# Kernel optimization log

Hardware: AMD Instinct MI355X
Metric: run time of the kernel (lower is better)

## Reference

```python
import jax, jax.numpy as jnp
import numpy as np

N = 100000
E = 3200000


def setup_inputs() -> dict:
    key = jax.random.key(0)
    ks = jax.random.split(key, 12)
    x = jax.random.normal(ks[0], (N, 124), dtype=jnp.float32)
    pos = jax.random.normal(ks[1], (N, 3), dtype=jnp.float32)
    z = jax.random.normal(ks[2], (N,), dtype=jnp.float32)
    edge_index = jax.random.randint(ks[3], (2, E), 0, N, dtype=jnp.int64)
    def lin(k, fin, fout):
        kw, kb = jax.random.split(k)
        s = 1.0 / np.sqrt(fin)
        W = jax.random.uniform(kw, (fin, fout), minval=-s, maxval=s, dtype=jnp.float32)
        b = jax.random.uniform(kb, (fout,), minval=-s, maxval=s, dtype=jnp.float32)
        return W, b
    W1, b1 = lin(ks[4], 128, 256)
    W2, b2 = lin(ks[5], 256, 256)
    W3, b3 = lin(ks[6], 256, 256)
    W4, b4 = lin(ks[7], 256, 1)
    return {"x": x, "pos": pos, "z": z, "edge_index": edge_index,
            "W1": W1, "b1": b1, "W2": W2, "b2": b2,
            "W3": W3, "b3": b3, "W4": W4, "b4": b4}


def reference(x, pos, z, edge_index, W1, b1, W2, b2, W3, b3, W4, b4):
    # features = hstack(x, pos, z[:, None])  -> [N, input_dim]
    feats = jnp.concatenate([x, pos, z[:, None]], axis=1)
    src, dst = edge_index[0], edge_index[1]
    # sum of neighbor (dst) features into each src node: O(E) segment-sum
    sums = jax.ops.segment_sum(feats[dst], src, num_segments=feats.shape[0])
    # per-node L2 normalize (matches torch.linalg.norm per row)
    h = sums / jnp.linalg.norm(sums, axis=1, keepdims=True)
    h = jax.nn.relu(h @ W1 + b1)
    h = jax.nn.relu(h @ W2 + b2)
    h = jax.nn.relu(h @ W3 + b3)
    h = h @ W4 + b4            # [N, 1]
    return jnp.mean(h, axis=0)  # [1]
```

## Files before the change

kernel.cpp:

```cpp
#include <hip/hip_runtime.h>
#include <math.h>

#define N_NODES 100000
#define N_EDGES 3200000
#define BSHIFT 6
#define NBUCK 1563
#define NBLK_E 256
#define EPB 12500
#define CAP 3072

typedef _Float16 half8 __attribute__((ext_vector_type(8)));
typedef float f32x4 __attribute__((ext_vector_type(4)));
typedef float f32x2 __attribute__((ext_vector_type(2)));

__device__ __forceinline__ void gload16(const void* gsrc, void* ldst) {
    __builtin_amdgcn_global_load_lds(
        (const __attribute__((address_space(1))) unsigned int*)gsrc,
        (__attribute__((address_space(3))) unsigned int*)ldst,
        16, 0, 0);
}

__global__ __launch_bounds__(256) void pack_kernel(
    const float* __restrict__ x, const float* __restrict__ pos,
    const float* __restrict__ z, unsigned int* __restrict__ feats8)
{
    int idx = blockIdx.x * blockDim.x + threadIdx.x;
    if (idx >= N_NODES * 32) return;
    int n = idx >> 5, j = idx & 31;
    float v[4];
    #pragma unroll
    for (int k = 0; k < 4; ++k) {
        int f = j * 4 + k;
        if (f < 124)      v[k] = x[n * 124 + f];
        else if (f < 127) v[k] = pos[n * 3 + (f - 124)];
        else              v[k] = z[n];
    }
    int u = 0;
    u = __builtin_amdgcn_cvt_pk_fp8_f32(v[0], v[1], u, false);
    u = __builtin_amdgcn_cvt_pk_fp8_f32(v[2], v[3], u, true);
    feats8[idx] = (unsigned int)u;
}

__global__ __launch_bounds__(256) void wprep_kernel(
    const float* __restrict__ W, int K, _Float16* __restrict__ WT)
{
    int idx = blockIdx.x * blockDim.x + threadIdx.x;
    if (idx >= K * 256) return;
    int k = idx >> 8, c = idx & 255;
    WT[c * K + k] = (_Float16)W[idx];
}

__global__ __launch_bounds__(1024) void coarse_hist_kernel(
    const int* __restrict__ ei, int* __restrict__ gcnt)
{
    __shared__ int bins[NBUCK];
    int t = threadIdx.x, blk = blockIdx.x;
    for (int b = t; b < NBUCK; b += 1024) bins[b] = 0;
    __syncthreads();
    int base = blk * EPB;
    for (int i = t; i < EPB; i += 1024) {
        int src = __builtin_nontemporal_load(&ei[base + i]);
        atomicAdd(&bins[src >> BSHIFT], 1);
    }
    __syncthreads();
    for (int b = t; b < NBUCK; b += 1024)
        gcnt[blk * NBUCK + b] = bins[b];
}

__global__ __launch_bounds__(256) void bucket_tot_kernel(
    const int* __restrict__ gcnt, int* __restrict__ btot)
{
    __shared__ int red[4];
    int b = blockIdx.x, t = threadIdx.x;
    int s = gcnt[t * NBUCK + b];
    #pragma unroll
    for (int off = 32; off > 0; off >>= 1) s += __shfl_xor(s, off, 64);
    if ((t & 63) == 0) red[t >> 6] = s;
    __syncthreads();
    if (t == 0) btot[b] = red[0] + red[1] + red[2] + red[3];
}

__global__ __launch_bounds__(1024) void scan_buckets_kernel(
    const int* __restrict__ btot, int* __restrict__ bbase)
{
    __shared__ int s[1024];
    int t = threadIdx.x;
    int i0 = 2 * t, i1 = 2 * t + 1;
    int v0 = (i0 < NBUCK) ? btot[i0] : 0;
    int v1 = (i1 < NBUCK) ? btot[i1] : 0;
    int sum = v0 + v1;
    s[t] = sum;
    __syncthreads();
    for (int off = 1; off < 1024; off <<= 1) {
        int o = (t >= off) ? s[t - off] : 0;
        __syncthreads();
        s[t] += o;
        __syncthreads();
    }
    int excl = s[t] - sum;
    if (i0 < NBUCK) bbase[i0] = excl;
    if (i1 < NBUCK) bbase[i1] = excl + v0;
    if (i0 == NBUCK - 1) bbase[NBUCK] = excl + v0;
    if (i1 == NBUCK - 1) bbase[NBUCK] = excl + v0 + v1;
}

__global__ __launch_bounds__(256) void colscan_kernel(
    const int* __restrict__ gcnt, const int* __restrict__ bbase,
    int* __restrict__ gbase)
{
    __shared__ int s[NBLK_E];
    int b = blockIdx.x, t = threadIdx.x;
    int v = gcnt[t * NBUCK + b];
    s[t] = v;
    __syncthreads();
    for (int off = 1; off < NBLK_E; off <<= 1) {
        int o = (t >= off) ? s[t - off] : 0;
        __syncthreads();
        s[t] += o;
        __syncthreads();
    }
    gbase[t * NBUCK + b] = bbase[b] + s[t] - v;
}

__global__ __launch_bounds__(1024) void bucket_scatter_kernel(
    const int* __restrict__ ei, const int* __restrict__ gcnt,
    const int* __restrict__ gbase, unsigned int* __restrict__ bucketed)
{
    __shared__ unsigned int val[EPB];
    __shared__ int gd[EPB];
    __shared__ int cur[NBUCK];
    __shared__ int gofs[NBUCK];
    __shared__ int ssum[1024];

    int t = threadIdx.x, blk = blockIdx.x;

    int i0 = 2 * t, i1 = 2 * t + 1;
    int c0 = (i0 < NBUCK) ? gcnt[blk * NBUCK + i0] : 0;
    int c1 = (i1 < NBUCK) ? gcnt[blk * NBUCK + i1] : 0;
    int sum = c0 + c1;
    ssum[t] = sum;
    __syncthreads();
    for (int off = 1; off < 1024; off <<= 1) {
        int o = (t >= off) ? ssum[t - off] : 0;
        __syncthreads();
        ssum[t] += o;
        __syncthreads();
    }
    int excl = ssum[t] - sum;
    if (i0 < NBUCK) { cur[i0] = excl;      gofs[i0] = gbase[blk * NBUCK + i0] - excl; }
    if (i1 < NBUCK) { cur[i1] = excl + c0; gofs[i1] = gbase[blk * NBUCK + i1] - (excl + c0); }
    __syncthreads();

    int base = blk * EPB;
    for (int i = t; i < EPB; i += 1024) {
        int e = base + i;
        int src = __builtin_nontemporal_load(&ei[e]);
        int dst = __builtin_nontemporal_load(&ei[N_EDGES + e]);
        int b = src >> BSHIFT;
        int r = atomicAdd(&cur[b], 1);
        val[r] = (unsigned int)dst | ((unsigned int)(src & 63) << 17);
        gd[r] = gofs[b] + r;
    }
    __syncthreads();

    for (int i = t; i < EPB; i += 1024)
        bucketed[gd[i]] = val[i];
}

__global__ __launch_bounds__(256) void sortagg_kernel(
    const int* __restrict__ bbase, const unsigned int* __restrict__ bucketed,
    const unsigned int* __restrict__ feats8, _Float16* __restrict__ h0)
{
    __shared__ unsigned int srt[CAP];
    __shared__ int excl[64], cur[64];

    int t = threadIdx.x, b = blockIdx.x;
    int segs = bbase[b], cnt = bbase[b + 1] - segs;
    if (cnt > CAP) cnt = CAP;

    if (t < 64) cur[t] = 0;
    __syncthreads();

    for (int i = t; i < cnt; i += 256)
        atomicAdd(&cur[(bucketed[segs + i] >> 17) & 63], 1);
    __syncthreads();

    int v = (t < 64) ? cur[t] : 0;
    if (t < 64) excl[t] = v;
    __syncthreads();
    for (int off = 1; off < 64; off <<= 1) {
        int o = (t >= off && t < 64) ? excl[t - off] : 0;
        __syncthreads();
        if (t < 64) excl[t] += o;
        __syncthreads();
    }
    if (t < 64) { excl[t] -= v; cur[t] = excl[t]; }
    __syncthreads();

    for (int i = t; i < cnt; i += 256) {
        unsigned int p = bucketed[segs + i];
        int r = atomicAdd(&cur[(p >> 17) & 63], 1);
        if (r < CAP) srt[r] = p & 0x1FFFFu;
    }
    __syncthreads();

    int w = t >> 6, lane = t & 63;
    int h = lane >> 5, s = lane & 31;
    const unsigned int* fb = feats8 + s;

#define ACC4(U)                                                     \
    a01 += __builtin_amdgcn_cvt_pk_f32_fp8((U), false);             \
    a23 += __builtin_amdgcn_cvt_pk_f32_fp8((U), true);

    for (int j = 0; j < 16; ++j) {
        int nl = w * 16 + j;
        int node = b * 64 + nl;
        if (node >= N_NODES) break;
        int start = excl[nl], end = cur[nl];
        f32x2 a01 = {0.f, 0.f}, a23 = {0.f, 0.f};
        int i = start;
        for (; i + 24 <= end; i += 24) {
            unsigned int uu[12];
            #pragma unroll
            for (int q = 0; q < 12; ++q)
                uu[q] = fb[(long long)srt[i + 2 * q + h] * 32];
            #pragma unroll
            for (int q = 0; q < 12; ++q) { ACC4(uu[q]); }
        }
        for (; i + 8 <= end; i += 8) {
            unsigned int uu[4];
            #pragma unroll
            for (int q = 0; q < 4; ++q)
                uu[q] = fb[(long long)srt[i + 2 * q + h] * 32];
            #pragma unroll
            for (int q = 0; q < 4; ++q) { ACC4(uu[q]); }
        }
        for (; i + 2 <= end; i += 2) {
            unsigned int u = fb[(long long)srt[i + h] * 32];
            ACC4(u);
        }
        if (i < end && h == 0) {
            unsigned int u = fb[(long long)srt[i] * 32];
            ACC4(u);
        }
        float a0 = a01[0], a1 = a01[1], a2 = a23[0], a3 = a23[1];
        a0 += __shfl_xor(a0, 32, 64);
        a1 += __shfl_xor(a1, 32, 64);
        a2 += __shfl_xor(a2, 32, 64);
        a3 += __shfl_xor(a3, 32, 64);
        float ss = a0 * a0 + a1 * a1 + a2 * a2 + a3 * a3;
        #pragma unroll
        for (int off = 16; off > 0; off >>= 1) ss += __shfl_xor(ss, off, 64);
        float inv = 1.0f / sqrtf(ss);
        if (h == 0) {
            union { uint2 u; _Float16 f[4]; } o;
            o.f[0] = (_Float16)(a0 * inv); o.f[1] = (_Float16)(a1 * inv);
            o.f[2] = (_Float16)(a2 * inv); o.f[3] = (_Float16)(a3 * inv);
            *reinterpret_cast<uint2*>(&h0[(long long)node * 128 + s * 4]) = o.u;
        }
    }
#undef ACC4
}

__global__ __launch_bounds__(256, 2) void fused_mlp_kernel(
    const _Float16* __restrict__ h0,
    const _Float16* __restrict__ WT1,
    const float* __restrict__ b1,
    const _Float16* __restrict__ WT2,
    const float* __restrict__ b2,
    const _Float16* __restrict__ WT3,
    const float* __restrict__ b3,
    const float* __restrict__ W4,
    float* __restrict__ partials, int M)
{
    __shared__ __align__(16) _Float16 sA[8 * 2048];
    __shared__ __align__(16) _Float16 sB[3][8192];

    const int t = threadIdx.x;
    const int row0 = blockIdx.x * 64;

    const int ar = t >> 2, ap = t & 3;
    const int ag = ap ^ ((ar >> 1) & 3);
    int arow = row0 + ar; if (arow > M - 1) arow = M - 1;
    const _Float16* aSrc = h0 + (long long)arow * 128 + ag * 8;

    const int bc0 = t >> 2;
    const int gb = ap ^ ((bc0 >> 1) & 3);

    const int w = t >> 6, lane = t & 63;
    const int wr = w >> 1, wc = w & 1;
    const int lrow = lane & 15, g = lane >> 4;

    unsigned int offA[2], offB[8];
    #pragma unroll
    for (int rt = 0; rt < 2; ++rt) {
        int r = wr * 32 + rt * 16 + lrow;
        offA[rt] = r * 64 + (g ^ ((r >> 1) & 3)) * 16;
    }
    #pragma unroll
    for (int ct = 0; ct < 8; ++ct) {
        int cidx = wc * 128 + ct * 16 + lrow;
        offB[ct] = cidx * 64 + (g ^ ((cidx >> 1) & 3)) * 16;
    }

    float bb1[8], bb2[8], bb3[8], w4v[8];
    #pragma unroll
    for (int ct = 0; ct < 8; ++ct) {
        int col = wc * 128 + ct * 16 + lrow;
        bb1[ct] = b1[col]; bb2[ct] = b2[col];
        bb3[ct] = b3[col]; w4v[ct] = W4[col];
    }

    f32x4 acc[2][8];
    #pragma unroll
    for (int i = 0; i < 2; ++i)
        #pragma unroll
        for (int j = 0; j < 8; ++j)
            acc[i][j] = (f32x4){0.f, 0.f, 0.f, 0.f};

#define STG(WT, Kv, KC, BUF)                                                 \
    {                                                                        \
        _Pragma("unroll")                                                    \
        for (int j = 0; j < 4; ++j)                                          \
            gload16((WT) + (long long)(bc0 + j * 64) * (Kv) + gb * 8 +       \
                        (KC) * 32,                                           \
                    (char*)sB[BUF] + j * 4096 + t * 16);                     \
    }

#define WB(N)                                                                \
    asm volatile("s_waitcnt vmcnt(" #N ")" ::: "memory");                    \
    __builtin_amdgcn_s_barrier();                                            \
    __builtin_amdgcn_sched_barrier(0);

#define EB() __builtin_amdgcn_s_barrier();

#define SEAM()                                                               \
    asm volatile("s_waitcnt lgkmcnt(0)" ::: "memory");                       \
    __builtin_amdgcn_s_barrier();                                            \
    __builtin_amdgcn_sched_barrier(0);

#define STORE_ACTS(BB)                                                       \
    {                                                                        \
        _Pragma("unroll")                                                    \
        for (int ct = 0; ct < 8; ++ct) {                                     \
            int col = wc * 128 + ct * 16 + lrow;                             \
            float bb = (BB)[ct];                                             \
            int chk = col >> 5, kk = col & 31;                               \
            int kg = kk >> 3, ke = kk & 7;                                   \
            _Pragma("unroll")                                                \
            for (int rt = 0; rt < 2; ++rt) {                                 \
                _Pragma("unroll")                                            \
                for (int jj = 0; jj < 4; ++jj) {                             \
                    int rowl = wr * 32 + rt * 16 + g * 4 + jj;               \
                    int slot = kg ^ ((rowl >> 1) & 3);                       \
                    sA[chk * 2048 + rowl * 32 + slot * 8 + ke] =             \
                        (_Float16)fmaxf(acc[rt][ct][jj] + bb, 0.f);          \
                    acc[rt][ct][jj] = 0.f;                                   \
                }                                                            \
            }                                                                \
        }                                                                    \
    }

#define MFMA_CHUNK(KC, BUF)                                                  \
    {                                                                        \
        half8 a[2], bfr[8];                                                  \
        __builtin_amdgcn_s_setprio(1);                                       \
        _Pragma("unroll")                                                    \
        for (int rt = 0; rt < 2; ++rt)                                       \
            a[rt] = *reinterpret_cast<const half8*>(                         \
                (const char*)sA + (KC) * 4096 + offA[rt]);                   \
        _Pragma("unroll")                                                    \
        for (int ct = 0; ct < 8; ++ct)                                       \
            bfr[ct] = *reinterpret_cast<const half8*>(                       \
                (const char*)sB[BUF] + offB[ct]);                            \
        _Pragma("unroll")                                                    \
        for (int rt = 0; rt < 2; ++rt)                                       \
            _Pragma("unroll")                                                \
            for (int ct = 0; ct < 8; ++ct)                                   \
                acc[rt][ct] = __builtin_amdgcn_mfma_f32_16x16x32_f16(        \
                    a[rt], bfr[ct], acc[rt][ct], 0, 0, 0);                   \
        __builtin_amdgcn_s_setprio(0);                                       \
    }

    #pragma unroll
    for (int kc = 0; kc < 4; ++kc)
        gload16(aSrc + kc * 32, (char*)sA + kc * 4096 + t * 16);
    STG(WT1, 128, 0, 0) STG(WT1, 128, 1, 1)

    STG(WT1, 128, 2, 2)  WB(8)  MFMA_CHUNK(0, 0)  EB()
    STG(WT1, 128, 3, 0)  WB(8)  MFMA_CHUNK(1, 1)  EB()
    STG(WT2, 256, 0, 1)  WB(8)  MFMA_CHUNK(2, 2)  EB()
    STG(WT2, 256, 1, 2)  WB(8)  MFMA_CHUNK(3, 0)  EB()
    STORE_ACTS(bb1) SEAM()
    STG(WT2, 256, 2, 0)  WB(8)  MFMA_CHUNK(0, 1)  EB()
    STG(WT2, 256, 3, 1)  WB(8)  MFMA_CHUNK(1, 2)  EB()
    STG(WT2, 256, 4, 2)  WB(8)  MFMA_CHUNK(2, 0)  EB()
    STG(WT2, 256, 5, 0)  WB(8)  MFMA_CHUNK(3, 1)  EB()
    STG(WT2, 256, 6, 1)  WB(8)  MFMA_CHUNK(4, 2)  EB()
    STG(WT2, 256, 7, 2)  WB(8)  MFMA_CHUNK(5, 0)  EB()
    STG(WT3, 256, 0, 0)  WB(8)  MFMA_CHUNK(6, 1)  EB()
    STG(WT3, 256, 1, 1)  WB(8)  MFMA_CHUNK(7, 2)  EB()
    STORE_ACTS(bb2) SEAM()
    STG(WT3, 256, 2, 2)  WB(8)  MFMA_CHUNK(0, 0)  EB()
    STG(WT3, 256, 3, 0)  WB(8)  MFMA_CHUNK(1, 1)  EB()
    STG(WT3, 256, 4, 1)  WB(8)  MFMA_CHUNK(2, 2)  EB()
    STG(WT3, 256, 5, 2)  WB(8)  MFMA_CHUNK(3, 0)  EB()
    STG(WT3, 256, 6, 0)  WB(8)  MFMA_CHUNK(4, 1)  EB()
    STG(WT3, 256, 7, 1)  WB(8)  MFMA_CHUNK(5, 2)  EB()
                         WB(4)  MFMA_CHUNK(6, 0)  EB()
                         WB(0)  MFMA_CHUNK(7, 1)  EB()

    float sum = 0.f;
    #pragma unroll
    for (int ct = 0; ct < 8; ++ct) {
        float bb = bb3[ct];
        float w4 = w4v[ct];
        #pragma unroll
        for (int rt = 0; rt < 2; ++rt) {
            #pragma unroll
            for (int jj = 0; jj < 4; ++jj) {
                int row = row0 + wr * 32 + rt * 16 + g * 4 + jj;
                if (row < M) {
                    float vv = fmaxf(acc[rt][ct][jj] + bb, 0.f);
                    sum += vv * w4;
                }
            }
        }
    }
    #pragma unroll
    for (int off = 32; off > 0; off >>= 1) sum += __shfl_xor(sum, off, 64);
    float* redf = reinterpret_cast<float*>(sA);
    if (lane == 0) redf[w] = sum;
    __syncthreads();
    if (t == 0) partials[blockIdx.x] = redf[0] + redf[1] + redf[2] + redf[3];
#undef STG
#undef WB
#undef EB
#undef SEAM
#undef STORE_ACTS
#undef MFMA_CHUNK
}

__global__ __launch_bounds__(256) void final_kernel(
    const float* __restrict__ partials, int n,
    const float* __restrict__ b4, float* __restrict__ out)
{
    __shared__ float buf[256];
    float s = 0.f;
    for (int i = threadIdx.x; i < n; i += 256) s += partials[i];
    buf[threadIdx.x] = s;
    __syncthreads();
    for (int off = 128; off > 0; off >>= 1) {
        if (threadIdx.x < off) buf[threadIdx.x] += buf[threadIdx.x + off];
        __syncthreads();
    }
    if (threadIdx.x == 0) out[0] = buf[0] / (float)N_NODES + b4[0];
}

extern "C" void kernel_launch(void* const* d_in, const int* in_sizes, int n_in,
                              void* d_out, int out_size, void* d_ws, size_t ws_size,
                              hipStream_t stream)
{
    const float* x   = (const float*)d_in[0];
    const float* pos = (const float*)d_in[1];
    const float* z   = (const float*)d_in[2];
    const int*   ei  = (const int*)d_in[3];
    const float* W1  = (const float*)d_in[4];
    const float* b1  = (const float*)d_in[5];
    const float* W2  = (const float*)d_in[6];
    const float* b2  = (const float*)d_in[7];
    const float* W3  = (const float*)d_in[8];
    const float* b3  = (const float*)d_in[9];
    const float* W4  = (const float*)d_in[10];
    const float* b4  = (const float*)d_in[11];
    float* out = (float*)d_out;

    char* ws = (char*)d_ws;
    unsigned int* feats8   = (unsigned int*)(ws);
    _Float16*     h0       = (_Float16*)    (ws + 12800000);
    int*          gcnt     = (int*)         (ws + 38400000);
    int*          gbase    = (int*)         (ws + 40000512);
    int*          btot     = (int*)         (ws + 41601024);
    int*          bbase    = (int*)         (ws + 41607276);
    unsigned int* bucketed = (unsigned int*)(ws + 41613532);
    _Float16*     WT1      = (_Float16*)    (ws + 54413568);
    _Float16*     WT2      = (_Float16*)    (ws + 54479104);
    _Float16*     WT3      = (_Float16*)    (ws + 54610176);
    float*        partials = (float*)       (ws + 54741248);

    const int gblocks = (N_NODES + 63) / 64;

    wprep_kernel<<<(128 * 256 + 255) / 256, 256, 0, stream>>>(W1, 128, WT1);
    wprep_kernel<<<(256 * 256 + 255) / 256, 256, 0, stream>>>(W2, 256, WT2);
    wprep_kernel<<<(256 * 256 + 255) / 256, 256, 0, stream>>>(W3, 256, WT3);

    pack_kernel<<<(N_NODES * 32 + 255) / 256, 256, 0, stream>>>(x, pos, z, feats8);

    coarse_hist_kernel<<<NBLK_E, 1024, 0, stream>>>(ei, gcnt);
    bucket_tot_kernel<<<NBUCK, 256, 0, stream>>>(gcnt, btot);
    scan_buckets_kernel<<<1, 1024, 0, stream>>>(btot, bbase);
    colscan_kernel<<<NBUCK, 256, 0, stream>>>(gcnt, bbase, gbase);
    bucket_scatter_kernel<<<NBLK_E, 1024, 0, stream>>>(ei, gcnt, gbase, bucketed);

    sortagg_kernel<<<NBUCK, 256, 0, stream>>>(bbase, bucketed, feats8, h0);

    fused_mlp_kernel<<<gblocks, 256, 0, stream>>>(
        h0, WT1, b1, WT2, b2, WT3, b3, W4, partials, N_NODES);

    final_kernel<<<1, 256, 0, stream>>>(partials, gblocks, b4, out);
}
```

Measured before the change: 179.2 us.

## Enlarge MLP row tile to 96, double-buffer weights, merge weight prep kernels

The fused MLP kernel now processes 96 rows per block instead of 64, so each staged weight chunk is reused across three 16-row MFMA tiles per wave rather than two. Weight staging drops from triple to double buffering, with adjusted wait counts. The three weight transpose/convert launches become a single kernel. The larger tile cuts weight traffic and block count, but raises accumulator registers and LDS use, and the shallower prefetch may expose more load latency.

Result: faster. 173.1 us (-3.4%).

```diff
diff --git a/kernel.cpp b/kernel.cpp
--- a/kernel.cpp
+++ b/kernel.cpp
@@ -8,6 +8,8 @@
 #define NBLK_E 256
 #define EPB 12500
 #define CAP 3072
+#define BM 96
+#define MLP_BLOCKS ((N_NODES + BM - 1) / BM)
 
 typedef _Float16 half8 __attribute__((ext_vector_type(8)));
 typedef float f32x4 __attribute__((ext_vector_type(4)));
@@ -41,13 +43,24 @@
     feats8[idx] = (unsigned int)u;
 }
 
-__global__ __launch_bounds__(256) void wprep_kernel(
-    const float* __restrict__ W, int K, _Float16* __restrict__ WT)
+__global__ __launch_bounds__(256) void wprep_all_kernel(
+    const float* __restrict__ W1, _Float16* __restrict__ WT1,
+    const float* __restrict__ W2, _Float16* __restrict__ WT2,
+    const float* __restrict__ W3, _Float16* __restrict__ WT3)
 {
     int idx = blockIdx.x * blockDim.x + threadIdx.x;
-    if (idx >= K * 256) return;
-    int k = idx >> 8, c = idx & 255;
-    WT[c * K + k] = (_Float16)W[idx];
+    if (idx < 128 * 256) {
+        int k = idx >> 8, c = idx & 255;
+        WT1[c * 128 + k] = (_Float16)W1[idx];
+    } else if (idx < 128 * 256 + 256 * 256) {
+        int i = idx - 128 * 256;
+        int k = i >> 8, c = i & 255;
+        WT2[c * 256 + k] = (_Float16)W2[i];
+    } else if (idx < 128 * 256 + 2 * 256 * 256) {
+        int i = idx - 128 * 256 - 256 * 256;
+        int k = i >> 8, c = i & 255;
+        WT3[c * 256 + k] = (_Float16)W3[i];
+    }
 }
 
 __global__ __launch_bounds__(1024) void coarse_hist_kernel(
@@ -273,28 +286,33 @@
     const float* __restrict__ W4,
     float* __restrict__ partials, int M)
 {
-    __shared__ __align__(16) _Float16 sA[8 * 2048];
-    __shared__ __align__(16) _Float16 sB[3][8192];
+    __shared__ __align__(16) _Float16 sA[8 * 3072];
+    __shared__ __align__(16) _Float16 sB[2][8192];
 
     const int t = threadIdx.x;
-    const int row0 = blockIdx.x * 64;
-
-    const int ar = t >> 2, ap = t & 3;
-    const int ag = ap ^ ((ar >> 1) & 3);
-    int arow = row0 + ar; if (arow > M - 1) arow = M - 1;
-    const _Float16* aSrc = h0 + (long long)arow * 128 + ag * 8;
+    const int row0 = blockIdx.x * BM;
+
+    const int ap0 = t & 3;
+    const int r0 = t >> 2;
+    const int ag0 = ap0 ^ ((r0 >> 1) & 3);
+    int arow0 = row0 + r0; if (arow0 > M - 1) arow0 = M - 1;
+    const _Float16* aSrc0 = h0 + (long long)arow0 * 128 + ag0 * 8;
+    const int r1 = (256 + t) >> 2;
+    const int ag1 = ap0 ^ ((r1 >> 1) & 3);
+    int arow1 = row0 + r1; if (arow1 > M - 1) arow1 = M - 1;
+    const _Float16* aSrc1 = h0 + (long long)arow1 * 128 + ag1 * 8;
 
     const int bc0 = t >> 2;
-    const int gb = ap ^ ((bc0 >> 1) & 3);
+    const int gb = ap0 ^ ((bc0 >> 1) & 3);
 
     const int w = t >> 6, lane = t & 63;
     const int wr = w >> 1, wc = w & 1;
     const int lrow = lane & 15, g = lane >> 4;
 
-    unsigned int offA[2], offB[8];
-    #pragma unroll
-    for (int rt = 0; rt < 2; ++rt) {
-        int r = wr * 32 + rt * 16 + lrow;
+    unsigned int offA[3], offB[8];
+    #pragma unroll
+    for (int rt = 0; rt < 3; ++rt) {
+        int r = wr * 48 + rt * 16 + lrow;
         offA[rt] = r * 64 + (g ^ ((r >> 1) & 3)) * 16;
     }
     #pragma unroll
@@ -311,9 +329,9 @@
         bb3[ct] = b3[col]; w4v[ct] = W4[col];
     }
 
-    f32x4 acc[2][8];
-    #pragma unroll
-    for (int i = 0; i < 2; ++i)
+    f32x4 acc[3][8];
+    #pragma unroll
+    for (int i = 0; i < 3; ++i)
         #pragma unroll
         for (int j = 0; j < 8; ++j)
             acc[i][j] = (f32x4){0.f, 0.f, 0.f, 0.f};
@@ -348,12 +366,12 @@
             int chk = col >> 5, kk = col & 31;                               \
             int kg = kk >> 3, ke = kk & 7;                                   \
             _Pragma("unroll")                                                \
-            for (int rt = 0; rt < 2; ++rt) {                                 \
+            for (int rt = 0; rt < 3; ++rt) {                                 \
                 _Pragma("unroll")                                            \
                 for (int jj = 0; jj < 4; ++jj) {                             \
-                    int rowl = wr * 32 + rt * 16 + g * 4 + jj;               \
+                    int rowl = wr * 48 + rt * 16 + g * 4 + jj;               \
                     int slot = kg ^ ((rowl >> 1) & 3);                       \
-                    sA[chk * 2048 + rowl * 32 + slot * 8 + ke] =             \
+                    sA[chk * 3072 + rowl * 32 + slot * 8 + ke] =             \
                         (_Float16)fmaxf(acc[rt][ct][jj] + bb, 0.f);          \
                     acc[rt][ct][jj] = 0.f;                                   \
                 }                                                            \
@@ -363,18 +381,18 @@
 
 #define MFMA_CHUNK(KC, BUF)                                                  \
     {                                                                        \
-        half8 a[2], bfr[8];                                                  \
+        half8 a[3], bfr[8];                                                  \
         __builtin_amdgcn_s_setprio(1);                                       \
         _Pragma("unroll")                                                    \
-        for (int rt = 0; rt < 2; ++rt)                                       \
+        for (int rt = 0; rt < 3; ++rt)                                       \
             a[rt] = *reinterpret_cast<const half8*>(                         \
-                (const char*)sA + (KC) * 4096 + offA[rt]);                   \
+                (const char*)sA + (KC) * 6144 + offA[rt]);                   \
         _Pragma("unroll")                                                    \
         for (int ct = 0; ct < 8; ++ct)                                       \
             bfr[ct] = *reinterpret_cast<const half8*>(                       \
                 (const char*)sB[BUF] + offB[ct]);                            \
         _Pragma("unroll")                                                    \
-        for (int rt = 0; rt < 2; ++rt)                                       \
+        for (int rt = 0; rt < 3; ++rt)                                       \
             _Pragma("unroll")                                                \
             for (int ct = 0; ct < 8; ++ct)                                   \
                 acc[rt][ct] = __builtin_amdgcn_mfma_f32_16x16x32_f16(        \
@@ -383,31 +401,34 @@
     }
 
     #pragma unroll
-    for (int kc = 0; kc < 4; ++kc)
-        gload16(aSrc + kc * 32, (char*)sA + kc * 4096 + t * 16);
-    STG(WT1, 128, 0, 0) STG(WT1, 128, 1, 1)
-
-    STG(WT1, 128, 2, 2)  WB(8)  MFMA_CHUNK(0, 0)  EB()
-    STG(WT1, 128, 3, 0)  WB(8)  MFMA_CHUNK(1, 1)  EB()
-    STG(WT2, 256, 0, 1)  WB(8)  MFMA_CHUNK(2, 2)  EB()
-    STG(WT2, 256, 1, 2)  WB(8)  MFMA_CHUNK(3, 0)  EB()
+    for (int kc = 0; kc < 4; ++kc) {
+        gload16(aSrc0 + kc * 32, (char*)sA + kc * 6144 + t * 16);
+        if (t < 128)
+            gload16(aSrc1 + kc * 32, (char*)sA + kc * 6144 + 4096 + t * 16);
+    }
+    STG(WT1, 128, 0, 0)
+
+    STG(WT1, 128, 1, 1)  WB(4)  MFMA_CHUNK(0, 0)  EB()
+    STG(WT1, 128, 2, 0)  WB(4)  MFMA_CHUNK(1, 1)  EB()
+    STG(WT1, 128, 3, 1)  WB(4)  MFMA_CHUNK(2, 0)  EB()
+    STG(WT2, 256, 0, 0)  WB(4)  MFMA_CHUNK(3, 1)  EB()
     STORE_ACTS(bb1) SEAM()
-    STG(WT2, 256, 2, 0)  WB(8)  MFMA_CHUNK(0, 1)  EB()
-    STG(WT2, 256, 3, 1)  WB(8)  MFMA_CHUNK(1, 2)  EB()
-    STG(WT2, 256, 4, 2)  WB(8)  MFMA_CHUNK(2, 0)  EB()
-    STG(WT2, 256, 5, 0)  WB(8)  MFMA_CHUNK(3, 1)  EB()
-    STG(WT2, 256, 6, 1)  WB(8)  MFMA_CHUNK(4, 2)  EB()
-    STG(WT2, 256, 7, 2)  WB(8)  MFMA_CHUNK(5, 0)  EB()
-    STG(WT3, 256, 0, 0)  WB(8)  MFMA_CHUNK(6, 1)  EB()
-    STG(WT3, 256, 1, 1)  WB(8)  MFMA_CHUNK(7, 2)  EB()
+    STG(WT2, 256, 1, 1)  WB(4)  MFMA_CHUNK(0, 0)  EB()
+    STG(WT2, 256, 2, 0)  WB(4)  MFMA_CHUNK(1, 1)  EB()
+    STG(WT2, 256, 3, 1)  WB(4)  MFMA_CHUNK(2, 0)  EB()
+    STG(WT2, 256, 4, 0)  WB(4)  MFMA_CHUNK(3, 1)  EB()
+    STG(WT2, 256, 5, 1)  WB(4)  MFMA_CHUNK(4, 0)  EB()
+    STG(WT2, 256, 6, 0)  WB(4)  MFMA_CHUNK(5, 1)  EB()
+    STG(WT2, 256, 7, 1)  WB(4)  MFMA_CHUNK(6, 0)  EB()
+    STG(WT3, 256, 0, 0)  WB(4)  MFMA_CHUNK(7, 1)  EB()
     STORE_ACTS(bb2) SEAM()
-    STG(WT3, 256, 2, 2)  WB(8)  MFMA_CHUNK(0, 0)  EB()
-    STG(WT3, 256, 3, 0)  WB(8)  MFMA_CHUNK(1, 1)  EB()
-    STG(WT3, 256, 4, 1)  WB(8)  MFMA_CHUNK(2, 2)  EB()
-    STG(WT3, 256, 5, 2)  WB(8)  MFMA_CHUNK(3, 0)  EB()
-    STG(WT3, 256, 6, 0)  WB(8)  MFMA_CHUNK(4, 1)  EB()
-    STG(WT3, 256, 7, 1)  WB(8)  MFMA_CHUNK(5, 2)  EB()
-                         WB(4)  MFMA_CHUNK(6, 0)  EB()
+    STG(WT3, 256, 1, 1)  WB(4)  MFMA_CHUNK(0, 0)  EB()
+    STG(WT3, 256, 2, 0)  WB(4)  MFMA_CHUNK(1, 1)  EB()
+    STG(WT3, 256, 3, 1)  WB(4)  MFMA_CHUNK(2, 0)  EB()
+    STG(WT3, 256, 4, 0)  WB(4)  MFMA_CHUNK(3, 1)  EB()
+    STG(WT3, 256, 5, 1)  WB(4)  MFMA_CHUNK(4, 0)  EB()
+    STG(WT3, 256, 6, 0)  WB(4)  MFMA_CHUNK(5, 1)  EB()
+    STG(WT3, 256, 7, 1)  WB(4)  MFMA_CHUNK(6, 0)  EB()
                          WB(0)  MFMA_CHUNK(7, 1)  EB()
 
     float sum = 0.f;
@@ -416,10 +437,10 @@
         float bb = bb3[ct];
         float w4 = w4v[ct];
         #pragma unroll
-        for (int rt = 0; rt < 2; ++rt) {
+        for (int rt = 0; rt < 3; ++rt) {
             #pragma unroll
             for (int jj = 0; jj < 4; ++jj) {
-                int row = row0 + wr * 32 + rt * 16 + g * 4 + jj;
+                int row = row0 + wr * 48 + rt * 16 + g * 4 + jj;
                 if (row < M) {
                     float vv = fmaxf(acc[rt][ct][jj] + bb, 0.f);
                     sum += vv * w4;
@@ -488,11 +509,8 @@
     _Float16*     WT3      = (_Float16*)    (ws + 54610176);
     float*        partials = (float*)       (ws + 54741248);
 
-    const int gblocks = (N_NODES + 63) / 64;
-
-    wprep_kernel<<<(128 * 256 + 255) / 256, 256, 0, stream>>>(W1, 128, WT1);
-    wprep_kernel<<<(256 * 256 + 255) / 256, 256, 0, stream>>>(W2, 256, WT2);
-    wprep_kernel<<<(256 * 256 + 255) / 256, 256, 0, stream>>>(W3, 256, WT3);
+    wprep_all_kernel<<<(128 * 256 + 2 * 256 * 256 + 255) / 256, 256, 0, stream>>>(
+        W1, WT1, W2, WT2, W3, WT3);
 
     pack_kernel<<<(N_NODES * 32 + 255) / 256, 256, 0, stream>>>(x, pos, z, feats8);
 
@@ -504,8 +522,8 @@
 
     sortagg_kernel<<<NBUCK, 256, 0, stream>>>(bbase, bucketed, feats8, h0);
 
-    fused_mlp_kernel<<<gblocks, 256, 0, stream>>>(
+    fused_mlp_kernel<<<MLP_BLOCKS, 256, 0, stream>>>(
         h0, WT1, b1, WT2, b2, WT3, b3, W4, partials, N_NODES);
 
-    final_kernel<<<1, 256, 0, stream>>>(partials, gblocks, b4, out);
-}
+    final_kernel<<<1, 256, 0, stream>>>(partials, MLP_BLOCKS, b4, out);
+}
```
